# Kernel tuning notes

Measured on AMD Instinct MI355X. Metric: run time of the kernel, lower is better.

## Reference

```python
import jax, jax.numpy as jnp
import numpy as np

NUM_HEADS = 32
NUM_KV_HEADS = 8
HEAD_DIM = 128
SCALE = 0.08838834764831845  # head_dim ** -0.5
LENS = [1024, 900, 800, 700, 600, 500, 400, 300]  # ragged sequence lengths


def setup_inputs() -> dict:
    key = jax.random.key(0)
    kq, kk, kv = jax.random.split(key, 3)
    cu = np.concatenate([[0], np.cumsum(LENS)]).astype(np.int32)
    T = int(cu[-1])  # 5224 total tokens
    q = jax.random.normal(kq, (T, NUM_HEADS * HEAD_DIM), jnp.float32)
    k = jax.random.normal(kk, (T, NUM_KV_HEADS * HEAD_DIM), jnp.float32)
    v = jax.random.normal(kv, (T, NUM_KV_HEADS * HEAD_DIM), jnp.float32)
    return {"q": q, "k": k, "v": v, "cu_seqlens": jnp.asarray(cu), "max_seqlen": 1024}


def _varlen_indices(cu_seqlens, total_tokens):
    # For each flat token, which sequence it belongs to and its position within it.
    pos = jnp.arange(total_tokens)
    seq_idx = jnp.searchsorted(cu_seqlens[1:], pos, side='right')
    pos_idx = pos - cu_seqlens[seq_idx]
    return seq_idx, pos_idx


def reference(q, k, v, cu_seqlens, max_seqlen):
    T = q.shape[0]
    B = cu_seqlens.shape[0] - 1
    q = q.reshape(T, NUM_HEADS, HEAD_DIM)
    k = k.reshape(T, NUM_KV_HEADS, HEAD_DIM)
    v = v.reshape(T, NUM_KV_HEADS, HEAD_DIM)
    si, pi = _varlen_indices(cu_seqlens, T)

    # varlen -> padded [B, L, H, D] (scatter)
    def pad(x):
        return jnp.zeros((B, max_seqlen) + x.shape[1:], x.dtype).at[si, pi].set(x)

    qp, kp, vp = pad(q), pad(k), pad(v)

    # GQA: repeat_interleave KV heads to match query heads
    rep = NUM_HEADS // NUM_KV_HEADS
    kp = jnp.repeat(kp, rep, axis=2)
    vp = jnp.repeat(vp, rep, axis=2)

    # causal SDPA on padded tensors
    scores = jnp.einsum('bihd,bjhd->bhij', qp, kp) * SCALE  # [B,H,L,L]
    causal = jnp.tril(jnp.ones((max_seqlen, max_seqlen), bool))
    scores = jnp.where(causal, scores, -jnp.inf)
    attn = jax.nn.softmax(scores, axis=-1)
    op = jnp.einsum('bhij,bjhd->bihd', attn, vp)  # [B,L,H,D]

    # padded -> varlen [T, H, D] (gather)
    return op[si, pi]
```

## Files before the change

kernel.cpp:

```cpp
#include <hip/hip_runtime.h>
#include <math.h>

#define NUM_HEADS 32
#define NUM_KV_HEADS 8
#define HEAD_DIM 128
#define QSTRIDE 4096
#define KSTRIDE 1024
#define SCALE 0.08838834764831845f
#define BM 128
#define BN 64
#define PSP 72
#define K1C (SCALE * 1.4426950408889634f)
#define K2C (6.0f * 1.4426950408889634f)

typedef __attribute__((ext_vector_type(8))) short short8;
typedef __attribute__((ext_vector_type(16))) float floatx16;

__device__ __forceinline__ ushort f2bf(float f) {
  union { float f; unsigned u; } x; x.f = f;
  unsigned r = x.u + 0x7fffu + ((x.u >> 16) & 1u);
  return (ushort)(r >> 16);
}

__device__ __forceinline__ void async16(ushort* lds, const ushort* g) {
  __builtin_amdgcn_global_load_lds(
      (const __attribute__((address_space(1))) unsigned*)g,
      (__attribute__((address_space(3))) unsigned*)lds, 16, 0, 0);
}

__global__ __launch_bounds__(256)
void prep_k(const float* __restrict__ k, ushort* __restrict__ kb, long n) {
  long i = ((long)blockIdx.x * 256 + threadIdx.x) * 8;
  if (i >= n) return;
  float4 a = *(const float4*)(k + i);
  float4 b = *(const float4*)(k + i + 4);
  ushort w[8] = {f2bf(a.x), f2bf(a.y), f2bf(a.z), f2bf(a.w),
                 f2bf(b.x), f2bf(b.y), f2bf(b.z), f2bf(b.w)};
  *(short8*)(kb + i) = *(short8*)w;
}

__global__ __launch_bounds__(256)
void prep_v(const float* __restrict__ v, ushort* __restrict__ vt, int T, int Tpad) {
  const int kt = blockIdx.x * 64;
  const int kvh = blockIdx.y;
  __shared__ __align__(16) ushort Ls[128][PSP];
  const int j = threadIdx.x >> 2;
  const int dc = (threadIdx.x & 3) * 32;
  const int t = kt + j;
  const int pj = (j & 31) * 2 + (j >> 5);
  const float* gv = v + (size_t)t * KSTRIDE + kvh * HEAD_DIM + dc;
  #pragma unroll
  for (int i = 0; i < 32; i += 4) {
    float4 x = (t < T) ? *(const float4*)(gv + i) : make_float4(0.f, 0.f, 0.f, 0.f);
    Ls[dc + i + 0][pj] = f2bf(x.x);
    Ls[dc + i + 1][pj] = f2bf(x.y);
    Ls[dc + i + 2][pj] = f2bf(x.z);
    Ls[dc + i + 3][pj] = f2bf(x.w);
  }
  __syncthreads();
  const int d = threadIdx.x >> 1;
  const int k0 = (threadIdx.x & 1) * 32;
  ushort* g = vt + (size_t)(kvh * HEAD_DIM + d) * Tpad + kt + k0;
  #pragma unroll
  for (int i = 0; i < 32; i += 8)
    *(short8*)(g + i) = *(short8*)&Ls[d][k0 + i];
}

__global__ __launch_bounds__(256, 2)
void fa_kernel(const float* __restrict__ q, const ushort* __restrict__ kb,
               const ushort* __restrict__ vt, const int* __restrict__ cu,
               float* __restrict__ out, int T, int Tpad, int B, int nt) {
  const int tid = threadIdx.x;
  const int wave = tid >> 6;
  const int lane = tid & 63;
  const int l32 = lane & 31;
  const int half = lane >> 5;
  const int xr = l32 & 7;
  const int h = blockIdx.y;
  const int kvh = h >> 2;
  const int tile = nt - 1 - blockIdx.x;
  const int row0 = tile * BM;

  __shared__ __align__(16) ushort KsL[64 * 128];
  __shared__ __align__(16) ushort VtL[128 * 64];
  __shared__ __align__(16) ushort PsL[4 * 32 * PSP];
  __shared__ int rstart[BM], rtok[BM];

  if (tid < BM) {
    int t = row0 + tid;
    int st = 0, tkk = -1;
    if (t < T) {
      int s = 0;
      while (s < B - 1 && cu[s + 1] <= t) s++;
      st = cu[s]; tkk = t;
    }
    rstart[tid] = st; rtok[tid] = tkk;
  }

  short8 aq[8];
  {
    int myrow = row0 + wave * 32 + l32;
    if (myrow < T) {
      const float* gq = q + (size_t)myrow * QSTRIDE + h * HEAD_DIM + half * 8;
      #pragma unroll
      for (int s = 0; s < 8; s++) {
        float4 x = *(const float4*)(gq + s * 16);
        float4 y = *(const float4*)(gq + s * 16 + 4);
        ushort w[8] = {f2bf(x.x), f2bf(x.y), f2bf(x.z), f2bf(x.w),
                       f2bf(y.x), f2bf(y.y), f2bf(y.z), f2bf(y.w)};
        aq[s] = *(short8*)w;
      }
    } else {
      #pragma unroll
      for (int s = 0; s < 8; s++) aq[s] = (short8){0, 0, 0, 0, 0, 0, 0, 0};
    }
  }
  __syncthreads();

  int rs[16], tk[16];
  #pragma unroll
  for (int r = 0; r < 16; r++) {
    int qr = (r & 3) + 8 * (r >> 2) + 4 * half;
    rs[r] = rstart[wave * 32 + qr];
    tk[r] = rtok[wave * 32 + qr];
  }

  size_t koff[4], voff[4];
  ushort *kdst[4], *vdst[4];
  #pragma unroll
  for (int i = 0; i < 4; i++) {
    int c = wave * 4 + i;
    int r = c * 4 + (lane >> 4);
    int js = lane & 15;
    int j = (js & 8) | ((js ^ (r & 7)) & 7);
    koff[i] = (size_t)r * KSTRIDE + kvh * HEAD_DIM + j * 8;
    kdst[i] = KsL + c * 512;
    int d = c * 8 + (lane >> 3);
    int js2 = lane & 7;
    int j2 = js2 ^ (d & 7);
    voff[i] = (size_t)(kvh * HEAD_DIM + d) * Tpad + j2 * 8;
    vdst[i] = VtL + c * 512;
  }

  floatx16 o0 = {0.f,0.f,0.f,0.f,0.f,0.f,0.f,0.f,0.f,0.f,0.f,0.f,0.f,0.f,0.f,0.f};
  floatx16 o1 = o0, o2 = o0, o3 = o0, lsum = o0;
  const short8 vones = {16256,16256,16256,16256,16256,16256,16256,16256};

  const int kt0 = (rstart[0] / BN) * BN;
  const int tmax = min(row0 + BM - 1, T - 1);

  ushort* psw = PsL + wave * (32 * PSP) + half * (4 * PSP) + l32 * 2;
  const ushort* psr = PsL + wave * (32 * PSP) + l32 * PSP + half * 8;

  for (int kt = kt0; kt <= tmax; kt += BN) {
    __syncthreads();
    #pragma unroll
    for (int i = 0; i < 4; i++) async16(kdst[i], kb + (size_t)kt * KSTRIDE + koff[i]);
    #pragma unroll
    for (int i = 0; i < 4; i++) async16(vdst[i], vt + voff[i] + kt);
    __syncthreads();

    floatx16 c0 = {0.f,0.f,0.f,0.f,0.f,0.f,0.f,0.f,0.f,0.f,0.f,0.f,0.f,0.f,0.f,0.f};
    floatx16 c1 = c0;
    #pragma unroll
    for (int s = 0; s < 8; s++) {
      int j = 2 * s + half;
      int jsw = (j & 8) | ((j ^ xr) & 7);
      const short8 b0 = *(const short8*)&KsL[l32 * 128 + jsw * 8];
      const short8 b1 = *(const short8*)&KsL[l32 * 128 + jsw * 8 + 4096];
      c0 = __builtin_amdgcn_mfma_f32_32x32x16_bf16(aq[s], b0, c0, 0, 0, 0);
      c1 = __builtin_amdgcn_mfma_f32_32x32x16_bf16(aq[s], b1, c1, 0, 0, 0);
    }

    const int kj0 = kt + l32, kj1 = kt + 32 + l32;
    #pragma unroll
    for (int r = 0; r < 16; r++) {
      bool v0 = (kj0 >= rs[r]) & (kj0 <= tk[r]);
      bool v1 = (kj1 >= rs[r]) & (kj1 <= tk[r]);
      float p0 = v0 ? __builtin_amdgcn_exp2f(fmaf(c0[r], K1C, -K2C)) : 0.f;
      float p1 = v1 ? __builtin_amdgcn_exp2f(fmaf(c1[r], K1C, -K2C)) : 0.f;
      unsigned pk = __builtin_amdgcn_perm(__float_as_uint(p1), __float_as_uint(p0),
                                          0x07060302u);
      *(unsigned*)(psw + ((r & 3) + 8 * (r >> 2)) * PSP) = pk;
    }

    #pragma unroll
    for (int ka = 0; ka < 4; ka++) {
      const short8 ap = *(const short8*)(psr + ka * 16);
      lsum = __builtin_amdgcn_mfma_f32_32x32x16_bf16(ap, vones, lsum, 0, 0, 0);
      int j2 = (2 * ka + half) ^ xr;
      const short8 bv0 = *(const short8*)&VtL[l32 * 64 + j2 * 8];
      const short8 bv1 = *(const short8*)&VtL[2048 + l32 * 64 + j2 * 8];
      const short8 bv2 = *(const short8*)&VtL[4096 + l32 * 64 + j2 * 8];
      const short8 bv3 = *(const short8*)&VtL[6144 + l32 * 64 + j2 * 8];
      o0 = __builtin_amdgcn_mfma_f32_32x32x16_bf16(ap, bv0, o0, 0, 0, 0);
      o1 = __builtin_amdgcn_mfma_f32_32x32x16_bf16(ap, bv1, o1, 0, 0, 0);
      o2 = __builtin_amdgcn_mfma_f32_32x32x16_bf16(ap, bv2, o2, 0, 0, 0);
      o3 = __builtin_amdgcn_mfma_f32_32x32x16_bf16(ap, bv3, o3, 0, 0, 0);
    }
  }

  #pragma unroll
  for (int r = 0; r < 16; r++) {
    if (tk[r] < 0) continue;
    float inv = 1.f / lsum[r];
    float* go = out + (size_t)tk[r] * QSTRIDE + h * HEAD_DIM + l32;
    go[0]  = o0[r] * inv;
    go[32] = o1[r] * inv;
    go[64] = o2[r] * inv;
    go[96] = o3[r] * inv;
  }
}

extern "C" void kernel_launch(void* const* d_in, const int* in_sizes, int n_in,
                              void* d_out, int out_size, void* d_ws, size_t ws_size,
                              hipStream_t stream) {
  const float* q = (const float*)d_in[0];
  const float* k = (const float*)d_in[1];
  const float* v = (const float*)d_in[2];
  const int* cu = (const int*)d_in[3];
  float* out = (float*)d_out;
  int T = in_sizes[0] / QSTRIDE;
  int B = in_sizes[3] - 1;
  int Tpad = ((T + 63) / 64) * 64;

  ushort* kb = (ushort*)d_ws;
  ushort* vt = kb + (size_t)Tpad * 1024;

  long nk = (long)T * KSTRIDE;
  hipLaunchKernelGGL(prep_k, dim3((unsigned)((nk / 8 + 255) / 256)), dim3(256), 0, stream,
                     k, kb, nk);
  hipLaunchKernelGGL(prep_v, dim3(Tpad / 64, NUM_KV_HEADS), dim3(256), 0, stream,
                     v, vt, T, Tpad);
  int nt = (T + BM - 1) / BM;
  hipLaunchKernelGGL(fa_kernel, dim3(nt, NUM_HEADS), dim3(256), 0, stream,
                     q, kb, vt, cu, out, T, Tpad, B, nt);
}
```

Measured before the change: 263.0 us.

## Pre-swizzle K/V into MFMA fragment layout and load directly from global per wave

The prep kernels now write K and V in bf16 in the exact per-lane MFMA operand order, so the attention kernel reads B operands straight from global memory into registers. This removes the shared-memory K/V staging and the block-wide barriers. Each wave now iterates only over its own causal key range instead of the block's range. Unmasked tiles take a fast path with no per-element mask. The grid is reordered to heads-major and occupancy is raised to 3 blocks per SM. The cost is that K/V reuse across the 4 waves now depends on L1/L2 rather than LDS, and each wave issues its own global loads.

```diff
diff --git a/kernel.cpp b/kernel.cpp
--- a/kernel.cpp
+++ b/kernel.cpp
@@ -7,11 +7,11 @@
 #define QSTRIDE 4096
 #define KSTRIDE 1024
 #define SCALE 0.08838834764831845f
+#define K1C (SCALE * 1.4426950408889634f)
+#define K2C (6.0f * 1.4426950408889634f)
 #define BM 128
 #define BN 64
 #define PSP 72
-#define K1C (SCALE * 1.4426950408889634f)
-#define K2C (6.0f * 1.4426950408889634f)
 
 typedef __attribute__((ext_vector_type(8))) short short8;
 typedef __attribute__((ext_vector_type(16))) float floatx16;
@@ -22,69 +22,82 @@
   return (ushort)(r >> 16);
 }
 
-__device__ __forceinline__ void async16(ushort* lds, const ushort* g) {
-  __builtin_amdgcn_global_load_lds(
-      (const __attribute__((address_space(1))) unsigned*)g,
-      (__attribute__((address_space(3))) unsigned*)lds, 16, 0, 0);
-}
-
 __global__ __launch_bounds__(256)
-void prep_k(const float* __restrict__ k, ushort* __restrict__ kb, long n) {
-  long i = ((long)blockIdx.x * 256 + threadIdx.x) * 8;
-  if (i >= n) return;
-  float4 a = *(const float4*)(k + i);
-  float4 b = *(const float4*)(k + i + 4);
-  ushort w[8] = {f2bf(a.x), f2bf(a.y), f2bf(a.z), f2bf(a.w),
-                 f2bf(b.x), f2bf(b.y), f2bf(b.z), f2bf(b.w)};
-  *(short8*)(kb + i) = *(short8*)w;
+void prep_k2(const float* __restrict__ k, ushort* __restrict__ kb2, int T, int Tpad) {
+  const int blk = blockIdx.x;
+  const int kvh = blockIdx.y;
+  const int kt = blk * 32;
+  __shared__ __align__(16) ushort Ls[32][136];
+  const int t = threadIdx.x;
+  #pragma unroll
+  for (int i = 0; i < 4; i++) {
+    int fi = t + 256 * i;
+    int row = fi >> 5;
+    int c4 = (fi & 31) * 4;
+    int tok = kt + row;
+    float4 x = (tok < T)
+        ? *(const float4*)(k + (size_t)tok * KSTRIDE + kvh * HEAD_DIM + c4)
+        : make_float4(0.f, 0.f, 0.f, 0.f);
+    Ls[row][c4 + 0] = f2bf(x.x); Ls[row][c4 + 1] = f2bf(x.y);
+    Ls[row][c4 + 2] = f2bf(x.z); Ls[row][c4 + 3] = f2bf(x.w);
+  }
+  __syncthreads();
+  ushort* outb = kb2 + ((size_t)kvh * (Tpad / 32) + blk) * 4096;
+  #pragma unroll
+  for (int i = 0; i < 2; i++) {
+    int c = t + 256 * i;
+    int s = c >> 6, hf = (c >> 5) & 1, l = c & 31;
+    *(short8*)(outb + c * 8) = *(short8*)&Ls[l][s * 16 + hf * 8];
+  }
 }
 
 __global__ __launch_bounds__(256)
-void prep_v(const float* __restrict__ v, ushort* __restrict__ vt, int T, int Tpad) {
-  const int kt = blockIdx.x * 64;
+void prep_v2(const float* __restrict__ v, ushort* __restrict__ vt2, int T, int Tpad) {
+  const int blk = blockIdx.x;
   const int kvh = blockIdx.y;
-  __shared__ __align__(16) ushort Ls[128][PSP];
-  const int j = threadIdx.x >> 2;
-  const int dc = (threadIdx.x & 3) * 32;
-  const int t = kt + j;
-  const int pj = (j & 31) * 2 + (j >> 5);
-  const float* gv = v + (size_t)t * KSTRIDE + kvh * HEAD_DIM + dc;
-  #pragma unroll
-  for (int i = 0; i < 32; i += 4) {
-    float4 x = (t < T) ? *(const float4*)(gv + i) : make_float4(0.f, 0.f, 0.f, 0.f);
-    Ls[dc + i + 0][pj] = f2bf(x.x);
-    Ls[dc + i + 1][pj] = f2bf(x.y);
-    Ls[dc + i + 2][pj] = f2bf(x.z);
-    Ls[dc + i + 3][pj] = f2bf(x.w);
+  const int kt = blk * 64;
+  __shared__ __align__(16) ushort Ls[128][72];
+  const int t = threadIdx.x;
+  {
+    int j = t >> 2, dc = (t & 3) * 32;
+    int tok = kt + j;
+    int pj = (j & 31) * 2 + (j >> 5);
+    const float* gv = v + (size_t)tok * KSTRIDE + kvh * HEAD_DIM + dc;
+    #pragma unroll
+    for (int i = 0; i < 32; i += 4) {
+      float4 x = (tok < T) ? *(const float4*)(gv + i) : make_float4(0.f, 0.f, 0.f, 0.f);
+      Ls[dc + i + 0][pj] = f2bf(x.x);
+      Ls[dc + i + 1][pj] = f2bf(x.y);
+      Ls[dc + i + 2][pj] = f2bf(x.z);
+      Ls[dc + i + 3][pj] = f2bf(x.w);
+    }
   }
   __syncthreads();
-  const int d = threadIdx.x >> 1;
-  const int k0 = (threadIdx.x & 1) * 32;
-  ushort* g = vt + (size_t)(kvh * HEAD_DIM + d) * Tpad + kt + k0;
-  #pragma unroll
-  for (int i = 0; i < 32; i += 8)
-    *(short8*)(g + i) = *(short8*)&Ls[d][k0 + i];
-}
-
-__global__ __launch_bounds__(256, 2)
-void fa_kernel(const float* __restrict__ q, const ushort* __restrict__ kb,
-               const ushort* __restrict__ vt, const int* __restrict__ cu,
-               float* __restrict__ out, int T, int Tpad, int B, int nt) {
+  ushort* outb = vt2 + ((size_t)kvh * (Tpad / 64) + blk) * 8192;
+  #pragma unroll
+  for (int i = 0; i < 4; i++) {
+    int c = t + 256 * i;
+    int db = c >> 8, ka = (c >> 6) & 3, hf = (c >> 5) & 1, l = c & 31;
+    *(short8*)(outb + c * 8) = *(short8*)&Ls[db * 32 + l][ka * 16 + hf * 8];
+  }
+}
+
+__global__ __launch_bounds__(256, 3)
+void fa_kernel(const float* __restrict__ q, const ushort* __restrict__ kb2,
+               const ushort* __restrict__ vt2, const int* __restrict__ cu,
+               float* __restrict__ out, int T, int Tpad, int B) {
   const int tid = threadIdx.x;
   const int wave = tid >> 6;
   const int lane = tid & 63;
   const int l32 = lane & 31;
   const int half = lane >> 5;
-  const int xr = l32 & 7;
-  const int h = blockIdx.y;
+  const int h = blockIdx.x;
   const int kvh = h >> 2;
-  const int tile = nt - 1 - blockIdx.x;
-  const int row0 = tile * BM;
-
-  __shared__ __align__(16) ushort KsL[64 * 128];
-  __shared__ __align__(16) ushort VtL[128 * 64];
+  const int row0 = blockIdx.y * BM;
+  const int base = row0 + wave * 32;
+
   __shared__ __align__(16) ushort PsL[4 * 32 * PSP];
-  __shared__ int rstart[BM], rtok[BM];
+  __shared__ int rstart[BM], rtok_v[BM];
 
   if (tid < BM) {
     int t = row0 + tid;
@@ -94,12 +107,13 @@
       while (s < B - 1 && cu[s + 1] <= t) s++;
       st = cu[s]; tkk = t;
     }
-    rstart[tid] = st; rtok[tid] = tkk;
-  }
+    rstart[tid] = st; rtok_v[tid] = tkk;
+  }
+  __syncthreads();
 
   short8 aq[8];
   {
-    int myrow = row0 + wave * 32 + l32;
+    int myrow = base + l32;
     if (myrow < T) {
       const float* gq = q + (size_t)myrow * QSTRIDE + h * HEAD_DIM + half * 8;
       #pragma unroll
@@ -115,96 +129,94 @@
       for (int s = 0; s < 8; s++) aq[s] = (short8){0, 0, 0, 0, 0, 0, 0, 0};
     }
   }
-  __syncthreads();
-
-  int rs[16], tk[16];
+
+  int rs[16];
   #pragma unroll
   for (int r = 0; r < 16; r++) {
     int qr = (r & 3) + 8 * (r >> 2) + 4 * half;
     rs[r] = rstart[wave * 32 + qr];
-    tk[r] = rtok[wave * 32 + qr];
-  }
-
-  size_t koff[4], voff[4];
-  ushort *kdst[4], *vdst[4];
-  #pragma unroll
-  for (int i = 0; i < 4; i++) {
-    int c = wave * 4 + i;
-    int r = c * 4 + (lane >> 4);
-    int js = lane & 15;
-    int j = (js & 8) | ((js ^ (r & 7)) & 7);
-    koff[i] = (size_t)r * KSTRIDE + kvh * HEAD_DIM + j * 8;
-    kdst[i] = KsL + c * 512;
-    int d = c * 8 + (lane >> 3);
-    int js2 = lane & 7;
-    int j2 = js2 ^ (d & 7);
-    voff[i] = (size_t)(kvh * HEAD_DIM + d) * Tpad + j2 * 8;
-    vdst[i] = VtL + c * 512;
-  }
+  }
+  const int rs0 = rstart[wave * 32];
+  const bool uniform = (base + 31 < T) && (rs0 == rstart[wave * 32 + 31]);
 
   floatx16 o0 = {0.f,0.f,0.f,0.f,0.f,0.f,0.f,0.f,0.f,0.f,0.f,0.f,0.f,0.f,0.f,0.f};
   floatx16 o1 = o0, o2 = o0, o3 = o0, lsum = o0;
   const short8 vones = {16256,16256,16256,16256,16256,16256,16256,16256};
 
-  const int kt0 = (rstart[0] / BN) * BN;
-  const int tmax = min(row0 + BM - 1, T - 1);
-
   ushort* psw = PsL + wave * (32 * PSP) + half * (4 * PSP) + l32 * 2;
   const ushort* psr = PsL + wave * (32 * PSP) + l32 * PSP + half * 8;
 
-  for (int kt = kt0; kt <= tmax; kt += BN) {
-    __syncthreads();
-    #pragma unroll
-    for (int i = 0; i < 4; i++) async16(kdst[i], kb + (size_t)kt * KSTRIDE + koff[i]);
-    #pragma unroll
-    for (int i = 0; i < 4; i++) async16(vdst[i], vt + voff[i] + kt);
-    __syncthreads();
-
-    floatx16 c0 = {0.f,0.f,0.f,0.f,0.f,0.f,0.f,0.f,0.f,0.f,0.f,0.f,0.f,0.f,0.f,0.f};
-    floatx16 c1 = c0;
-    #pragma unroll
-    for (int s = 0; s < 8; s++) {
-      int j = 2 * s + half;
-      int jsw = (j & 8) | ((j ^ xr) & 7);
-      const short8 b0 = *(const short8*)&KsL[l32 * 128 + jsw * 8];
-      const short8 b1 = *(const short8*)&KsL[l32 * 128 + jsw * 8 + 4096];
-      c0 = __builtin_amdgcn_mfma_f32_32x32x16_bf16(aq[s], b0, c0, 0, 0, 0);
-      c1 = __builtin_amdgcn_mfma_f32_32x32x16_bf16(aq[s], b1, c1, 0, 0, 0);
-    }
-
-    const int kj0 = kt + l32, kj1 = kt + 32 + l32;
-    #pragma unroll
-    for (int r = 0; r < 16; r++) {
-      bool v0 = (kj0 >= rs[r]) & (kj0 <= tk[r]);
-      bool v1 = (kj1 >= rs[r]) & (kj1 <= tk[r]);
-      float p0 = v0 ? __builtin_amdgcn_exp2f(fmaf(c0[r], K1C, -K2C)) : 0.f;
-      float p1 = v1 ? __builtin_amdgcn_exp2f(fmaf(c1[r], K1C, -K2C)) : 0.f;
-      unsigned pk = __builtin_amdgcn_perm(__float_as_uint(p1), __float_as_uint(p0),
-                                          0x07060302u);
-      *(unsigned*)(psw + ((r & 3) + 8 * (r >> 2)) * PSP) = pk;
-    }
-
-    #pragma unroll
-    for (int ka = 0; ka < 4; ka++) {
-      const short8 ap = *(const short8*)(psr + ka * 16);
-      lsum = __builtin_amdgcn_mfma_f32_32x32x16_bf16(ap, vones, lsum, 0, 0, 0);
-      int j2 = (2 * ka + half) ^ xr;
-      const short8 bv0 = *(const short8*)&VtL[l32 * 64 + j2 * 8];
-      const short8 bv1 = *(const short8*)&VtL[2048 + l32 * 64 + j2 * 8];
-      const short8 bv2 = *(const short8*)&VtL[4096 + l32 * 64 + j2 * 8];
-      const short8 bv3 = *(const short8*)&VtL[6144 + l32 * 64 + j2 * 8];
-      o0 = __builtin_amdgcn_mfma_f32_32x32x16_bf16(ap, bv0, o0, 0, 0, 0);
-      o1 = __builtin_amdgcn_mfma_f32_32x32x16_bf16(ap, bv1, o1, 0, 0, 0);
-      o2 = __builtin_amdgcn_mfma_f32_32x32x16_bf16(ap, bv2, o2, 0, 0, 0);
-      o3 = __builtin_amdgcn_mfma_f32_32x32x16_bf16(ap, bv3, o3, 0, 0, 0);
+  if (base < T) {
+    const int kt0 = (rs0 / BN) * BN;
+    const int tmaxw = min(base + 31, T - 1);
+    const size_t kvbase_k = (size_t)kvh * (Tpad / 32) * 4096;
+    const size_t kvbase_v = (size_t)kvh * (Tpad / 64) * 8192;
+
+    for (int kt = kt0; kt <= tmaxw; kt += BN) {
+      const ushort* kbase = kb2 + kvbase_k + (size_t)(kt >> 5) * 4096;
+      floatx16 c0 = {0.f,0.f,0.f,0.f,0.f,0.f,0.f,0.f,0.f,0.f,0.f,0.f,0.f,0.f,0.f,0.f};
+      floatx16 c1 = c0;
+      #pragma unroll
+      for (int s = 0; s < 8; s++) {
+        const int co = (s * 64 + half * 32 + l32) * 8;
+        const short8 b0 = *(const short8*)(kbase + co);
+        const short8 b1 = *(const short8*)(kbase + 4096 + co);
+        c0 = __builtin_amdgcn_mfma_f32_32x32x16_bf16(aq[s], b0, c0, 0, 0, 0);
+        c1 = __builtin_amdgcn_mfma_f32_32x32x16_bf16(aq[s], b1, c1, 0, 0, 0);
+      }
+
+      const bool fast = uniform && (kt >= rs0) && (kt + BN - 1 <= base);
+      if (fast) {
+        #pragma unroll
+        for (int r = 0; r < 16; r++) {
+          float p0 = __builtin_amdgcn_exp2f(fmaf(c0[r], K1C, -K2C));
+          float p1 = __builtin_amdgcn_exp2f(fmaf(c1[r], K1C, -K2C));
+          unsigned pk = __builtin_amdgcn_perm(__float_as_uint(p1), __float_as_uint(p0),
+                                              0x07060302u);
+          *(unsigned*)(psw + ((r & 3) + 8 * (r >> 2)) * PSP) = pk;
+        }
+      } else {
+        const int kj0 = kt + l32, kj1 = kt + 32 + l32;
+        #pragma unroll
+        for (int r = 0; r < 16; r++) {
+          int qr = (r & 3) + 8 * (r >> 2) + 4 * half;
+          int tok = base + qr;
+          bool rowv = tok < T;
+          bool v0 = rowv & (kj0 >= rs[r]) & (kj0 <= tok);
+          bool v1 = rowv & (kj1 >= rs[r]) & (kj1 <= tok);
+          float p0 = v0 ? __builtin_amdgcn_exp2f(fmaf(c0[r], K1C, -K2C)) : 0.f;
+          float p1 = v1 ? __builtin_amdgcn_exp2f(fmaf(c1[r], K1C, -K2C)) : 0.f;
+          unsigned pk = __builtin_amdgcn_perm(__float_as_uint(p1), __float_as_uint(p0),
+                                              0x07060302u);
+          *(unsigned*)(psw + ((r & 3) + 8 * (r >> 2)) * PSP) = pk;
+        }
+      }
+
+      const ushort* vbase = vt2 + kvbase_v + (size_t)(kt >> 6) * 8192;
+      #pragma unroll
+      for (int ka = 0; ka < 4; ka++) {
+        const short8 ap = *(const short8*)(psr + ka * 16);
+        lsum = __builtin_amdgcn_mfma_f32_32x32x16_bf16(ap, vones, lsum, 0, 0, 0);
+        const int vo = (ka * 2 + half) * 32 + l32;
+        const short8 bv0 = *(const short8*)(vbase + (vo) * 8);
+        const short8 bv1 = *(const short8*)(vbase + (vo + 256) * 8);
+        const short8 bv2 = *(const short8*)(vbase + (vo + 512) * 8);
+        const short8 bv3 = *(const short8*)(vbase + (vo + 768) * 8);
+        o0 = __builtin_amdgcn_mfma_f32_32x32x16_bf16(ap, bv0, o0, 0, 0, 0);
+        o1 = __builtin_amdgcn_mfma_f32_32x32x16_bf16(ap, bv1, o1, 0, 0, 0);
+        o2 = __builtin_amdgcn_mfma_f32_32x32x16_bf16(ap, bv2, o2, 0, 0, 0);
+        o3 = __builtin_amdgcn_mfma_f32_32x32x16_bf16(ap, bv3, o3, 0, 0, 0);
+      }
     }
   }
 
   #pragma unroll
   for (int r = 0; r < 16; r++) {
-    if (tk[r] < 0) continue;
+    int qr = (r & 3) + 8 * (r >> 2) + 4 * half;
+    int tok = base + qr;
+    if (tok >= T) continue;
     float inv = 1.f / lsum[r];
-    float* go = out + (size_t)tk[r] * QSTRIDE + h * HEAD_DIM + l32;
+    float* go = out + (size_t)tok * QSTRIDE + h * HEAD_DIM + l32;
     go[0]  = o0[r] * inv;
     go[32] = o1[r] * inv;
     go[64] = o2[r] * inv;
@@ -224,15 +236,14 @@
   int B = in_sizes[3] - 1;
   int Tpad = ((T + 63) / 64) * 64;
 
-  ushort* kb = (ushort*)d_ws;
-  ushort* vt = kb + (size_t)Tpad * 1024;
-
-  long nk = (long)T * KSTRIDE;
-  hipLaunchKernelGGL(prep_k, dim3((unsigned)((nk / 8 + 255) / 256)), dim3(256), 0, stream,
-                     k, kb, nk);
-  hipLaunchKernelGGL(prep_v, dim3(Tpad / 64, NUM_KV_HEADS), dim3(256), 0, stream,
-                     v, vt, T, Tpad);
+  ushort* kb2 = (ushort*)d_ws;
+  ushort* vt2 = kb2 + (size_t)Tpad * 1024;
+
+  hipLaunchKernelGGL(prep_k2, dim3(Tpad / 32, NUM_KV_HEADS), dim3(256), 0, stream,
+                     k, kb2, T, Tpad);
+  hipLaunchKernelGGL(prep_v2, dim3(Tpad / 64, NUM_KV_HEADS), dim3(256), 0, stream,
+                     v, vt2, T, Tpad);
   int nt = (T + BM - 1) / BM;
-  hipLaunchKernelGGL(fa_kernel, dim3(nt, NUM_HEADS), dim3(256), 0, stream,
-                     q, kb, vt, cu, out, T, Tpad, B, nt);
-}
+  hipLaunchKernelGGL(fa_kernel, dim3(NUM_HEADS, nt), dim3(256), 0, stream,
+                     q, kb2, vt2, cu, out, T, Tpad, B);
+}
```

Result: slower. 390.4 us (+48.4%).
